# Kernel tuning notes

Hardware: AMD Instinct MI355X
Metric: run time of the kernel (lower is better)

## Reference

```python
import jax, jax.numpy as jnp
import numpy as np

HID = 2048      # hidden_size
NH = 32         # num query heads
NKV = 8         # num kv heads
HD = HID // NH  # head_dim = 64
E = 4           # num_experts
N = 2048        # flattened token count (divisible by E)
THETA = 10000.0
EPS = 1e-6


def setup_inputs() -> dict:
    key = jax.random.key(0)
    ks = jax.random.split(key, 8)
    s = HID ** -0.5
    return {
        "hidden_states": jax.random.normal(ks[0], (N, HID), jnp.float32),
        "positions": jnp.arange(N, dtype=jnp.int32),
        "sort_idx": jax.random.permutation(ks[1], N).astype(jnp.int32),
        "q_proj_w": jax.random.normal(ks[2], (E, HID, NH * HD), jnp.float32) * s,
        "o_proj_w": jax.random.normal(ks[3], (E, NH * HD, HID), jnp.float32) * s,
        "k_w": jax.random.normal(ks[4], (HID, NKV * HD), jnp.float32) * s,
        "v_w": jax.random.normal(ks[5], (HID, NKV * HD), jnp.float32) * s,
        "q_norm_w": jnp.ones((HD,), jnp.float32),
        "k_norm_w": jnp.ones((HD,), jnp.float32),
    }


def _routed_proj(x, weight, sort_idx):
    # x: [N, din], weight: [E, din, dout], sort_idx: permutation of N
    n, din = x.shape
    e, _, dout = weight.shape
    chunk = n // e
    sorted_x = x[sort_idx].reshape(e, chunk, din)          # gather + split
    sorted_out = jnp.einsum('ecd,edo->eco', sorted_x, weight).reshape(n, dout)
    return jnp.zeros((n, dout), sorted_out.dtype).at[sort_idx].set(sorted_out)


def _rms_norm(x, w):
    # x: [N, H, D] normalized over last dim
    var = jnp.mean(jnp.square(x), axis=-1, keepdims=True)
    return x * jax.lax.rsqrt(var + EPS) * w


def _rope_neox(x, positions):
    # x: [N, H, D]
    half = HD // 2
    inv_freq = 1.0 / (THETA ** (jnp.arange(0, HD, 2, dtype=jnp.float32) / HD))  # [D/2]
    freqs = positions.astype(jnp.float32)[:, None] * inv_freq                   # [N, D/2]
    cos = jnp.cos(freqs)[:, None, :]  # [N,1,D/2]
    sin = jnp.sin(freqs)[:, None, :]
    x1, x2 = x[..., :half], x[..., half:]
    return jnp.concatenate([x1 * cos - x2 * sin, x2 * cos + x1 * sin], axis=-1)


def reference(hidden_states, positions, sort_idx, q_proj_w, o_proj_w, k_w, v_w,
              q_norm_w, k_norm_w):
    n = hidden_states.shape[0]
    # projections
    q = _routed_proj(hidden_states, q_proj_w, sort_idx)        # [N, NH*HD]
    k = hidden_states @ k_w                                    # [N, NKV*HD]
    v = hidden_states @ v_w                                    # [N, NKV*HD]
    # qk norm per head
    q = _rms_norm(q.reshape(n, NH, HD), q_norm_w)
    k = _rms_norm(k.reshape(n, NKV, HD), k_norm_w)
    # rotary (neox style)
    q = _rope_neox(q, positions)
    k = _rope_neox(k, positions)
    v = v.reshape(n, NKV, HD)
    # GQA causal attention over the packed sequence
    g = NH // NKV
    k_rep = jnp.repeat(k, g, axis=1)  # [N, NH, HD]
    v_rep = jnp.repeat(v, g, axis=1)
    scores = jnp.einsum('qhd,khd->hqk', q, k_rep) * (HD ** -0.5)
    causal = positions[:, None] >= positions[None, :]          # [N, N]
    scores = jnp.where(causal[None], scores, jnp.finfo(scores.dtype).min)
    attn = jax.nn.softmax(scores, axis=-1)
    o = jnp.einsum('hqk,khd->qhd', attn, v_rep).reshape(n, NH * HD)
    # routed output projection
    return _routed_proj(o, o_proj_w, sort_idx)
```

## Files before the change

### kernel.cpp

```cpp
#include <hip/hip_runtime.h>
#include <hip/hip_bf16.h>

#define N_TOK 2048
#define HID   2048
#define NH    32
#define NKV   8
#define HD    64
#define NEXP  4
#define CHUNK (N_TOK / NEXP)
#define KV_DIM (NKV * HD)

typedef __attribute__((ext_vector_type(8))) short short8;
typedef __attribute__((ext_vector_type(4))) float float4v;

__device__ inline short f2bf(float f) {
    __hip_bfloat16 h = __float2bfloat16(f);
    return *reinterpret_cast<short*>(&h);
}
__device__ inline float bf2f(short s) {
    __hip_bfloat16 h = *reinterpret_cast<__hip_bfloat16*>(&s);
    return __bfloat162float(h);
}
__device__ __forceinline__ float fast_exp2(float x) {
    float r;
    asm("v_exp_f32 %0, %1" : "=v"(r) : "v"(x));
    return r;
}

__device__ __forceinline__ void gld_lds16(const void* g, void* l) {
    __builtin_amdgcn_global_load_lds(
        (const __attribute__((address_space(1))) unsigned int*)g,
        (__attribute__((address_space(3))) unsigned int*)l, 16, 0, 0);
}

__device__ __forceinline__ void wtrans_tile(
    const float* __restrict__ in, short* __restrict__ out, int Nw,
    int k0, int n0, float (*T)[65], int t)
{
#pragma unroll
    for (int i = 0; i < 16; i++) {
        int idx = t + i * 256, kl = idx >> 6, nl = idx & 63;
        T[kl][nl] = in[(size_t)(k0 + kl) * Nw + n0 + nl];
    }
    __syncthreads();
#pragma unroll
    for (int i = 0; i < 2; i++) {
        int idx = t + i * 256;
        int nl = idx >> 3, k8 = (idx & 7) * 8;
        short8 s;
#pragma unroll
        for (int j = 0; j < 8; j++) s[j] = f2bf(T[k8 + j][nl]);
        *(short8*)&out[(size_t)(n0 + nl) * 2048 + k0 + k8] = s;
    }
}

__global__ __launch_bounds__(256)
void prep1(const float* __restrict__ hidden, const float* __restrict__ qw,
           const float* __restrict__ kw, const float* __restrict__ vw,
           short* __restrict__ Xbf, short* __restrict__ Wq,
           short* __restrict__ Wkv)
{
    __shared__ float T[64][65];
    const int b = blockIdx.x;
    const int t = threadIdx.x;

    if (b < 2048) {
        size_t i = (size_t)b * 256 + t;
        float4 a = ((const float4*)hidden)[i * 2];
        float4 c = ((const float4*)hidden)[i * 2 + 1];
        short8 s;
        s[0] = f2bf(a.x); s[1] = f2bf(a.y); s[2] = f2bf(a.z); s[3] = f2bf(a.w);
        s[4] = f2bf(c.x); s[5] = f2bf(c.y); s[6] = f2bf(c.z); s[7] = f2bf(c.w);
        ((short8*)Xbf)[i] = s;
    } else if (b < 6144) {
        int b2 = b - 2048;
        int k0 = (b2 & 31) * 64, n0 = ((b2 >> 5) & 31) * 64, e = b2 >> 10;
        wtrans_tile(qw + (size_t)e * 2048 * 2048, Wq + (size_t)e * 2048 * 2048,
                    2048, k0, n0, T, t);
    } else {
        int b3 = b - 6144;
        int k0 = (b3 & 31) * 64, n0 = ((b3 >> 5) & 7) * 64, z = b3 >> 8;
        wtrans_tile(z ? vw : kw, Wkv + (size_t)z * 512 * 2048, 512, k0, n0, T, t);
    }
}

__global__ __launch_bounds__(256)
void prep2(const float* __restrict__ ow, short* __restrict__ Wo,
           short* __restrict__ qb, short* __restrict__ kvb,
           const float* __restrict__ qnw, const float* __restrict__ knw,
           const int* __restrict__ positions, short* __restrict__ vt)
{
    __shared__ __align__(16) char smem[64 * 65 * 4];
    const int b = blockIdx.x;
    const int t = threadIdx.x;

    if (b < 4096) {
        float (*T)[65] = (float(*)[65])smem;
        int k0 = (b & 31) * 64, n0 = ((b >> 5) & 31) * 64, e = b >> 10;
        wtrans_tile(ow + (size_t)e * 2048 * 2048, Wo + (size_t)e * 2048 * 2048,
                    2048, k0, n0, T, t);
    } else if (b < 24576) {
        const int lane = t & 63, wave = t >> 6;
        int u = (b - 4096) * 4 + wave;
        int row = u / 40, h = u - row * 40;
        short* p;
        const float* w;
        float oscale;
        if (h < NH) { p = qb + (size_t)row * 2048 + h * HD + lane; w = qnw;
                      oscale = 0.125f * 1.44269504f; }
        else        { p = kvb + (size_t)row * 1024 + (h - NH) * HD + lane; w = knw;
                      oscale = 1.0f; }
        float x = bf2f(*p);
        float ss = x * x;
#pragma unroll
        for (int off = 32; off > 0; off >>= 1) ss += __shfl_xor(ss, off, 64);
        float rs = rsqrtf(ss * (1.0f / HD) + 1e-6f);
        float xn = x * rs * w[lane];
        int j = lane & 31;
        float inv_freq = fast_exp2(-(float)j * 0.41524101186f);
        float fr = (float)positions[row] * inv_freq;
        float c = __cosf(fr), s = __sinf(fr);
        float partner = __shfl_xor(xn, 32, 64);
        float o = (lane < 32) ? (xn * c - partner * s) : (xn * c + partner * s);
        *p = f2bf(o * oscale);
    } else {
        short (*T)[66] = (short(*)[66])smem;
        int b4 = b - 24576;
        int n0 = (b4 & 31) * 64, h = b4 >> 5;
#pragma unroll
        for (int i = 0; i < 16; i++) {
            int idx = t + i * 256, nl = idx >> 6, dl = idx & 63;
            T[nl][dl] = kvb[(size_t)(n0 + nl) * 1024 + 512 + h * HD + dl];
        }
        __syncthreads();
#pragma unroll
        for (int i = 0; i < 16; i++) {
            int idx = t + i * 256, dl = idx >> 6, nl = idx & 63;
            vt[((size_t)h * HD + dl) * N_TOK + n0 + nl] = T[nl][dl];
        }
    }
}

template <bool OUT_F32>
__device__ __forceinline__ void gemm_core(
    const short* __restrict__ X, const short* __restrict__ Wt,
    const int* __restrict__ sidx, void* __restrict__ OUT,
    int dout, bool routed, int bx, int by,
    short* As0, short* Bs0, short* As1, short* Bs1, int* ridx)
{
    const int t  = threadIdx.x;
    const int m0 = by * 128;
    const int n0 = bx * 128;

    if (t < 128) ridx[t] = routed ? sidx[m0 + t] : (m0 + t);
    __syncthreads();

    const short* Wb = Wt + (routed ? (size_t)(m0 / CHUNK) * (size_t)dout * 2048 : 0);

    const int seg = (t & 3) * 8;
    const short* ga0 = X  + (size_t)ridx[t >> 2] * 2048 + seg;
    const short* ga1 = X  + (size_t)ridx[64 + (t >> 2)] * 2048 + seg;
    const short* gb0 = Wb + (size_t)(n0 + (t >> 2)) * 2048 + seg;
    const short* gb1 = Wb + (size_t)(n0 + 64 + (t >> 2)) * 2048 + seg;

    const int lane = t & 63;
    const int wave = t >> 6;
    const int wl   = wave * 64 * 8;
    const int col  = lane & 15;
    const int rowg = lane >> 4;
    const int wm   = (wave >> 1) * 64;
    const int wn   = (wave & 1) * 64;

    int offA[4], offB[4];
#pragma unroll
    for (int i = 0; i < 4; i++) {
        offA[i] = (wm + i * 16 + col) * 32 + rowg * 8;
        offB[i] = (wn + i * 16 + col) * 32 + rowg * 8;
    }

    float4v acc[4][4];
#pragma unroll
    for (int mt = 0; mt < 4; mt++)
#pragma unroll
        for (int nt = 0; nt < 4; nt++) acc[mt][nt] = (float4v){0.f, 0.f, 0.f, 0.f};

    auto stage = [&](int k0, short* A, short* B) {
        gld_lds16(ga0 + k0, A + wl);
        gld_lds16(ga1 + k0, A + 256 * 8 + wl);
        gld_lds16(gb0 + k0, B + wl);
        gld_lds16(gb1 + k0, B + 256 * 8 + wl);
    };
    auto compute = [&](const short* A, const short* B) {
        short8 af[4], bfr[4];
#pragma unroll
        for (int i = 0; i < 4; i++) af[i] = *(const short8*)&A[offA[i]];
#pragma unroll
        for (int i = 0; i < 4; i++) bfr[i] = *(const short8*)&B[offB[i]];
#pragma unroll
        for (int mt = 0; mt < 4; mt++)
#pragma unroll
            for (int nt = 0; nt < 4; nt++)
                acc[mt][nt] = __builtin_amdgcn_mfma_f32_16x16x32_bf16(
                    af[mt], bfr[nt], acc[mt][nt], 0, 0, 0);
    };

    stage(0, As0, Bs0);
    asm volatile("s_waitcnt vmcnt(0)" ::: "memory");
    __builtin_amdgcn_s_barrier();

    for (int k0 = 0; k0 < 2048; k0 += 64) {
        stage(k0 + 32, As1, Bs1);
        compute(As0, Bs0);
        asm volatile("s_waitcnt vmcnt(0)" ::: "memory");
        __builtin_amdgcn_s_barrier();

        if (k0 + 64 < 2048) stage(k0 + 64, As0, Bs0);
        compute(As1, Bs1);
        asm volatile("s_waitcnt vmcnt(0)" ::: "memory");
        __builtin_amdgcn_s_barrier();
    }

#pragma unroll
    for (int mt = 0; mt < 4; mt++) {
#pragma unroll
        for (int r = 0; r < 4; r++) {
            int row = ridx[wm + mt * 16 + rowg * 4 + r];
#pragma unroll
            for (int nt = 0; nt < 4; nt++) {
                int colg = n0 + wn + nt * 16 + col;
                float v = acc[mt][nt][r];
                if (OUT_F32) ((float*)OUT)[(size_t)row * dout + colg] = v;
                else         ((short*)OUT)[(size_t)row * dout + colg] = f2bf(v);
            }
        }
    }
}

__global__ __launch_bounds__(256)
void gemm_qkv(const short* __restrict__ X, const short* __restrict__ Wq,
              const short* __restrict__ Wkv, const int* __restrict__ sidx,
              short* __restrict__ qout, short* __restrict__ kvout)
{
    __shared__ __align__(16) short As0[128 * 32], Bs0[128 * 32];
    __shared__ __align__(16) short As1[128 * 32], Bs1[128 * 32];
    __shared__ int ridx[128];
    int b = blockIdx.x;
    if (b < 256)
        gemm_core<false>(X, Wq, sidx, qout, 2048, true, b & 15, b >> 4,
                         As0, Bs0, As1, Bs1, ridx);
    else {
        b -= 256;
        gemm_core<false>(X, Wkv, nullptr, kvout, 1024, false, b & 7, b >> 3,
                         As0, Bs0, As1, Bs1, ridx);
    }
}

__global__ __launch_bounds__(256)
void gemm_o(const short* __restrict__ X, const short* __restrict__ Wt,
            const int* __restrict__ sidx, float* __restrict__ OUT)
{
    __shared__ __align__(16) short As0[128 * 32], Bs0[128 * 32];
    __shared__ __align__(16) short As1[128 * 32], Bs1[128 * 32];
    __shared__ int ridx[128];
    gemm_core<true>(X, Wt, sidx, OUT, 2048, true, blockIdx.x, blockIdx.y,
                    As0, Bs0, As1, Bs1, ridx);
}

__global__ __launch_bounds__(256)
void attn_mfma(const short* __restrict__ qb, const short* __restrict__ kb,
               const short* __restrict__ vt, const int* __restrict__ positions,
               short* __restrict__ ob)
{
    __shared__ __align__(16) short Ks[64][72];
    __shared__ __align__(16) short Vt[64][72];
    __shared__ __align__(16) short Ps[4][16][72];

    const int head = blockIdx.y;
    const int kvh  = head >> 2;
    const int t    = threadIdx.x;
    const int lane = t & 63;
    const int wave = t >> 6;
    const int rowg = lane >> 4;
    const int col  = lane & 15;

    const int sr = t >> 2;
    const int sc = (t & 3) * 16;
    const float BIAS = 9.0f * 1.44269504f;

#pragma unroll
    for (int pass = 0; pass < 2; pass++) {
        const int qt = pass == 0 ? (31 - (int)blockIdx.x) : (int)blockIdx.x;
        const int q0 = qt * 64;
        const int m0 = q0 + wave * 16;

        const short* qrow = qb + (size_t)(m0 + col) * HID + head * HD;
        short8 aq0 = *(const short8*)(qrow + rowg * 8);
        short8 aq1 = *(const short8*)(qrow + 32 + rowg * 8);

        int pq[4];
        float l_i[4];
#pragma unroll
        for (int r = 0; r < 4; r++) {
            pq[r] = positions[m0 + rowg * 4 + r];
            l_i[r] = 0.f;
        }
        float4v oacc[4];
#pragma unroll
        for (int n = 0; n < 4; n++) oacc[n] = (float4v){0.f, 0.f, 0.f, 0.f};

        const int nkt = qt + 1;
        for (int kt = 0; kt < nkt; kt++) {
            const int k0 = kt * 64;
            __syncthreads();
            {
                const short* kp = kb + (size_t)(k0 + sr) * 1024 + kvh * HD + sc;
                const short* vp = vt + ((size_t)kvh * HD + sr) * N_TOK + k0 + sc;
                short8 kA = *(const short8*)(kp);
                short8 kB = *(const short8*)(kp + 8);
                short8 vA = *(const short8*)(vp);
                short8 vB = *(const short8*)(vp + 8);
                *(short8*)&Ks[sr][sc]     = kA;
                *(short8*)&Ks[sr][sc + 8] = kB;
                *(short8*)&Vt[sr][sc]     = vA;
                *(short8*)&Vt[sr][sc + 8] = vB;
            }
            __syncthreads();

            float4v c[4];
#pragma unroll
            for (int j = 0; j < 4; j++) {
                short8 blo = *(const short8*)&Ks[j * 16 + col][rowg * 8];
                short8 bhi = *(const short8*)&Ks[j * 16 + col][32 + rowg * 8];
                float4v cc = (float4v){0.f, 0.f, 0.f, 0.f};
                cc = __builtin_amdgcn_mfma_f32_16x16x32_bf16(aq0, blo, cc, 0, 0, 0);
                cc = __builtin_amdgcn_mfma_f32_16x16x32_bf16(aq1, bhi, cc, 0, 0, 0);
                c[j] = cc;
            }

            if (kt == qt) {
#pragma unroll
                for (int j = 0; j < 4; j++) {
                    int pk = positions[k0 + j * 16 + col];
#pragma unroll
                    for (int r = 0; r < 4; r++)
                        if (pq[r] < pk) c[j][r] = -1e30f;
                }
            }

#pragma unroll
            for (int j = 0; j < 4; j++)
#pragma unroll
                for (int r = 0; r < 4; r++) {
                    float p = fast_exp2(c[j][r] - BIAS);
                    l_i[r] += p;
                    Ps[wave][rowg * 4 + r][j * 16 + col] = f2bf(p);
                }

            __asm__ volatile("s_waitcnt lgkmcnt(0)" ::: "memory");

            short8 ap0 = *(const short8*)&Ps[wave][col][rowg * 8];
            short8 ap1 = *(const short8*)&Ps[wave][col][32 + rowg * 8];
#pragma unroll
            for (int n = 0; n < 4; n++) {
                short8 blo = *(const short8*)&Vt[n * 16 + col][rowg * 8];
                short8 bhi = *(const short8*)&Vt[n * 16 + col][32 + rowg * 8];
                float4v a2 = oacc[n];
                a2 = __builtin_amdgcn_mfma_f32_16x16x32_bf16(ap0, blo, a2, 0, 0, 0);
                a2 = __builtin_amdgcn_mfma_f32_16x16x32_bf16(ap1, bhi, a2, 0, 0, 0);
                oacc[n] = a2;
            }
        }

#pragma unroll
        for (int r = 0; r < 4; r++) {
#pragma unroll
            for (int off = 1; off < 16; off <<= 1)
                l_i[r] += __shfl_xor(l_i[r], off, 64);
            l_i[r] = 1.f / l_i[r];
        }
#pragma unroll
        for (int n = 0; n < 4; n++)
#pragma unroll
            for (int r = 0; r < 4; r++)
                ob[(size_t)(m0 + rowg * 4 + r) * HID + head * HD + n * 16 + col] =
                    f2bf(oacc[n][r] * l_i[r]);
    }
}

extern "C" void kernel_launch(void* const* d_in, const int* in_sizes, int n_in,
                              void* d_out, int out_size, void* d_ws, size_t ws_size,
                              hipStream_t stream)
{
    (void)in_sizes; (void)n_in; (void)out_size; (void)ws_size;

    const float* hidden    = (const float*)d_in[0];
    const int*   positions = (const int*)  d_in[1];
    const int*   sort_idx  = (const int*)  d_in[2];
    const float* q_proj_w  = (const float*)d_in[3];
    const float* o_proj_w  = (const float*)d_in[4];
    const float* k_w       = (const float*)d_in[5];
    const float* v_w       = (const float*)d_in[6];
    const float* q_norm_w  = (const float*)d_in[7];
    const float* k_norm_w  = (const float*)d_in[8];
    float* out = (float*)d_out;

    const size_t M1 = 1024 * 1024;
    short* Wqo = (short*)d_ws;
    short* Wkv = Wqo + 16 * M1;
    short* Xbf = Wkv + 2 * M1;
    short* qb  = Xbf + 4 * M1;
    short* kvb = qb  + 4 * M1;
    short* vt  = kvb + 2 * M1;
    short* obf = Xbf;

    prep1<<<6656, 256, 0, stream>>>(hidden, q_proj_w, k_w, v_w, Xbf, Wqo, Wkv);

    gemm_qkv<<<384, 256, 0, stream>>>(Xbf, Wqo, Wkv, sort_idx, qb, kvb);

    prep2<<<24832, 256, 0, stream>>>(o_proj_w, Wqo, qb, kvb, q_norm_w, k_norm_w,
                                     positions, vt);

    attn_mfma<<<dim3(16, NH), 256, 0, stream>>>(qb, kvb, vt, positions, obf);

    gemm_o<<<dim3(16, 16), 256, 0, stream>>>(obf, Wqo, sort_idx, out);
}
```

Measured before the change: 334.2 us.

## Fuse QK norm, RoPE and V transpose into QKV GEMM epilogue; overlap Wo transpose with attention

The separate prep2 kernel is removed. RMS norm and RoPE for q and k now run in the QKV GEMM epilogue using cross-lane shuffles, and V is written directly in transposed layout. The o_proj weight transpose is merged into the attention launch as extra blocks so it overlaps with attention, and K/V tile loads are register-prefetched one iteration ahead. This removes a full read/write pass over q, k and v and one kernel launch, at the cost of a heavier GEMM epilogue and mixed block types in the attention grid.

```diff
diff --git a/kernel.cpp b/kernel.cpp
--- a/kernel.cpp
+++ b/kernel.cpp
@@ -8,10 +8,13 @@
 #define HD    64
 #define NEXP  4
 #define CHUNK (N_TOK / NEXP)
-#define KV_DIM (NKV * HD)
 
 typedef __attribute__((ext_vector_type(8))) short short8;
+typedef __attribute__((ext_vector_type(4))) short short4v;
 typedef __attribute__((ext_vector_type(4))) float float4v;
+
+#define QSCALE (0.125f * 1.44269504f)
+#define RLOG   0.41524101186f
 
 __device__ inline short f2bf(float f) {
     __hip_bfloat16 h = __float2bfloat16(f);
@@ -84,68 +87,13 @@
     }
 }
 
-__global__ __launch_bounds__(256)
-void prep2(const float* __restrict__ ow, short* __restrict__ Wo,
-           short* __restrict__ qb, short* __restrict__ kvb,
-           const float* __restrict__ qnw, const float* __restrict__ knw,
-           const int* __restrict__ positions, short* __restrict__ vt)
-{
-    __shared__ __align__(16) char smem[64 * 65 * 4];
-    const int b = blockIdx.x;
-    const int t = threadIdx.x;
-
-    if (b < 4096) {
-        float (*T)[65] = (float(*)[65])smem;
-        int k0 = (b & 31) * 64, n0 = ((b >> 5) & 31) * 64, e = b >> 10;
-        wtrans_tile(ow + (size_t)e * 2048 * 2048, Wo + (size_t)e * 2048 * 2048,
-                    2048, k0, n0, T, t);
-    } else if (b < 24576) {
-        const int lane = t & 63, wave = t >> 6;
-        int u = (b - 4096) * 4 + wave;
-        int row = u / 40, h = u - row * 40;
-        short* p;
-        const float* w;
-        float oscale;
-        if (h < NH) { p = qb + (size_t)row * 2048 + h * HD + lane; w = qnw;
-                      oscale = 0.125f * 1.44269504f; }
-        else        { p = kvb + (size_t)row * 1024 + (h - NH) * HD + lane; w = knw;
-                      oscale = 1.0f; }
-        float x = bf2f(*p);
-        float ss = x * x;
-#pragma unroll
-        for (int off = 32; off > 0; off >>= 1) ss += __shfl_xor(ss, off, 64);
-        float rs = rsqrtf(ss * (1.0f / HD) + 1e-6f);
-        float xn = x * rs * w[lane];
-        int j = lane & 31;
-        float inv_freq = fast_exp2(-(float)j * 0.41524101186f);
-        float fr = (float)positions[row] * inv_freq;
-        float c = __cosf(fr), s = __sinf(fr);
-        float partner = __shfl_xor(xn, 32, 64);
-        float o = (lane < 32) ? (xn * c - partner * s) : (xn * c + partner * s);
-        *p = f2bf(o * oscale);
-    } else {
-        short (*T)[66] = (short(*)[66])smem;
-        int b4 = b - 24576;
-        int n0 = (b4 & 31) * 64, h = b4 >> 5;
-#pragma unroll
-        for (int i = 0; i < 16; i++) {
-            int idx = t + i * 256, nl = idx >> 6, dl = idx & 63;
-            T[nl][dl] = kvb[(size_t)(n0 + nl) * 1024 + 512 + h * HD + dl];
-        }
-        __syncthreads();
-#pragma unroll
-        for (int i = 0; i < 16; i++) {
-            int idx = t + i * 256, dl = idx >> 6, nl = idx & 63;
-            vt[((size_t)h * HD + dl) * N_TOK + n0 + nl] = T[nl][dl];
-        }
-    }
-}
-
-template <bool OUT_F32>
+template <int EPI>
 __device__ __forceinline__ void gemm_core(
     const short* __restrict__ X, const short* __restrict__ Wt,
     const int* __restrict__ sidx, void* __restrict__ OUT,
     int dout, bool routed, int bx, int by,
+    const int* __restrict__ positions, const float* __restrict__ nw,
+    short* __restrict__ vt,
     short* As0, short* Bs0, short* As1, short* Bs1, int* ridx)
 {
     const int t  = threadIdx.x;
@@ -220,38 +168,98 @@
         __builtin_amdgcn_s_barrier();
     }
 
-#pragma unroll
-    for (int mt = 0; mt < 4; mt++) {
-#pragma unroll
-        for (int r = 0; r < 4; r++) {
-            int row = ridx[wm + mt * 16 + rowg * 4 + r];
+    if (EPI == 0) {
+#pragma unroll
+        for (int mt = 0; mt < 4; mt++)
+#pragma unroll
+            for (int r = 0; r < 4; r++) {
+                int row = ridx[wm + mt * 16 + rowg * 4 + r];
+#pragma unroll
+                for (int nt = 0; nt < 4; nt++)
+                    ((float*)OUT)[(size_t)row * dout + n0 + wn + nt * 16 + col] =
+                        acc[mt][nt][r];
+            }
+        return;
+    }
+
+    const bool is_v = (EPI == 2) && (n0 + wn >= 512);
+
+    if (is_v) {
+#pragma unroll
+        for (int mt = 0; mt < 4; mt++) {
+            int rowb = m0 + wm + mt * 16 + rowg * 4;
 #pragma unroll
             for (int nt = 0; nt < 4; nt++) {
-                int colg = n0 + wn + nt * 16 + col;
-                float v = acc[mt][nt][r];
-                if (OUT_F32) ((float*)OUT)[(size_t)row * dout + colg] = v;
-                else         ((short*)OUT)[(size_t)row * dout + colg] = f2bf(v);
+                int d = n0 + wn + nt * 16 + col - 512;
+                short4v sv;
+#pragma unroll
+                for (int r = 0; r < 4; r++) sv[r] = f2bf(acc[mt][nt][r]);
+                *(short4v*)&vt[(size_t)d * N_TOK + rowb] = sv;
             }
         }
+        return;
+    }
+
+    {
+        const int   h     = (n0 + wn) >> 6;
+        const float oscl  = (EPI == 1) ? QSCALE : 1.0f;
+        const int   ldo   = (EPI == 1) ? 2048 : 512;
+        short* ob = (short*)OUT;
+        float invf0 = fast_exp2(-(float)col * RLOG);
+        float invf1 = fast_exp2(-(float)(16 + col) * RLOG);
+        float wv[4];
+#pragma unroll
+        for (int nt = 0; nt < 4; nt++) wv[nt] = nw[nt * 16 + col];
+
+#pragma unroll
+        for (int mt = 0; mt < 4; mt++)
+#pragma unroll
+            for (int r = 0; r < 4; r++) {
+                int row = ridx[wm + mt * 16 + rowg * 4 + r];
+                float x0 = acc[mt][0][r], x1 = acc[mt][1][r];
+                float x2 = acc[mt][2][r], x3 = acc[mt][3][r];
+                float ss = x0 * x0 + x1 * x1 + x2 * x2 + x3 * x3;
+#pragma unroll
+                for (int off = 1; off < 16; off <<= 1)
+                    ss += __shfl_xor(ss, off, 64);
+                float rs = rsqrtf(ss * (1.0f / HD) + 1e-6f);
+                x0 *= rs * wv[0]; x1 *= rs * wv[1];
+                x2 *= rs * wv[2]; x3 *= rs * wv[3];
+                float pos = (float)positions[row];
+                float fr0 = pos * invf0, fr1 = pos * invf1;
+                float c0 = __cosf(fr0), s0 = __sinf(fr0);
+                float c1 = __cosf(fr1), s1 = __sinf(fr1);
+                float o0 = x0 * c0 - x2 * s0;
+                float o1 = x1 * c1 - x3 * s1;
+                float o2 = x2 * c0 + x0 * s0;
+                float o3 = x3 * c1 + x1 * s1;
+                size_t base = (size_t)row * ldo + h * 64 + col;
+                ob[base]      = f2bf(o0 * oscl);
+                ob[base + 16] = f2bf(o1 * oscl);
+                ob[base + 32] = f2bf(o2 * oscl);
+                ob[base + 48] = f2bf(o3 * oscl);
+            }
     }
 }
 
 __global__ __launch_bounds__(256)
 void gemm_qkv(const short* __restrict__ X, const short* __restrict__ Wq,
               const short* __restrict__ Wkv, const int* __restrict__ sidx,
-              short* __restrict__ qout, short* __restrict__ kvout)
+              short* __restrict__ qb, short* __restrict__ kb,
+              short* __restrict__ vt, const int* __restrict__ positions,
+              const float* __restrict__ qnw, const float* __restrict__ knw)
 {
     __shared__ __align__(16) short As0[128 * 32], Bs0[128 * 32];
     __shared__ __align__(16) short As1[128 * 32], Bs1[128 * 32];
     __shared__ int ridx[128];
     int b = blockIdx.x;
     if (b < 256)
-        gemm_core<false>(X, Wq, sidx, qout, 2048, true, b & 15, b >> 4,
-                         As0, Bs0, As1, Bs1, ridx);
+        gemm_core<1>(X, Wq, sidx, qb, 2048, true, b & 15, b >> 4,
+                     positions, qnw, nullptr, As0, Bs0, As1, Bs1, ridx);
     else {
         b -= 256;
-        gemm_core<false>(X, Wkv, nullptr, kvout, 1024, false, b & 7, b >> 3,
-                         As0, Bs0, As1, Bs1, ridx);
+        gemm_core<2>(X, Wkv, nullptr, kb, 1024, false, b & 7, b >> 3,
+                     positions, knw, vt, As0, Bs0, As1, Bs1, ridx);
     }
 }
 
@@ -262,22 +270,35 @@
     __shared__ __align__(16) short As0[128 * 32], Bs0[128 * 32];
     __shared__ __align__(16) short As1[128 * 32], Bs1[128 * 32];
     __shared__ int ridx[128];
-    gemm_core<true>(X, Wt, sidx, OUT, 2048, true, blockIdx.x, blockIdx.y,
-                    As0, Bs0, As1, Bs1, ridx);
+    gemm_core<0>(X, Wt, sidx, OUT, 2048, true, blockIdx.x, blockIdx.y,
+                 nullptr, nullptr, nullptr, As0, Bs0, As1, Bs1, ridx);
 }
 
 __global__ __launch_bounds__(256)
-void attn_mfma(const short* __restrict__ qb, const short* __restrict__ kb,
+void attn_plus(const short* __restrict__ qb, const short* __restrict__ kb,
                const short* __restrict__ vt, const int* __restrict__ positions,
-               short* __restrict__ ob)
-{
-    __shared__ __align__(16) short Ks[64][72];
-    __shared__ __align__(16) short Vt[64][72];
-    __shared__ __align__(16) short Ps[4][16][72];
-
-    const int head = blockIdx.y;
+               short* __restrict__ ob,
+               const float* __restrict__ ow, short* __restrict__ Wo)
+{
+    __shared__ __align__(16) char smem[27648];
+    const int b = blockIdx.x;
+    const int t = threadIdx.x;
+
+    if (b >= 512) {
+        float (*T)[65] = (float(*)[65])smem;
+        int b2 = b - 512;
+        int k0 = (b2 & 31) * 64, n0 = ((b2 >> 5) & 31) * 64, e = b2 >> 10;
+        wtrans_tile(ow + (size_t)e * 2048 * 2048, Wo + (size_t)e * 2048 * 2048,
+                    2048, k0, n0, T, t);
+        return;
+    }
+
+    short (*Ks)[72] = (short(*)[72])smem;
+    short (*Vt)[72] = (short(*)[72])(smem + 64 * 72 * 2);
+    short (*Ps)[72] = (short(*)[72])(smem + 2 * 64 * 72 * 2);
+
+    const int head = b >> 4;
     const int kvh  = head >> 2;
-    const int t    = threadIdx.x;
     const int lane = t & 63;
     const int wave = t >> 6;
     const int rowg = lane >> 4;
@@ -289,7 +310,7 @@
 
 #pragma unroll
     for (int pass = 0; pass < 2; pass++) {
-        const int qt = pass == 0 ? (31 - (int)blockIdx.x) : (int)blockIdx.x;
+        const int qt = pass == 0 ? (31 - (b & 15)) : (b & 15);
         const int q0 = qt * 64;
         const int m0 = q0 + wave * 16;
 
@@ -308,24 +329,34 @@
 #pragma unroll
         for (int n = 0; n < 4; n++) oacc[n] = (float4v){0.f, 0.f, 0.f, 0.f};
 
+        const short* kpb = kb + (size_t)sr * 512 + kvh * HD + sc;
+        const short* vpb = vt + ((size_t)kvh * HD + sr) * N_TOK + sc;
+
         const int nkt = qt + 1;
+        short8 kA, kB, vA, vB;
+        {
+            kA = *(const short8*)(kpb);
+            kB = *(const short8*)(kpb + 8);
+            vA = *(const short8*)(vpb);
+            vB = *(const short8*)(vpb + 8);
+        }
+
         for (int kt = 0; kt < nkt; kt++) {
+            __syncthreads();
+            *(short8*)&Ks[sr][sc]     = kA;
+            *(short8*)&Ks[sr][sc + 8] = kB;
+            *(short8*)&Vt[sr][sc]     = vA;
+            *(short8*)&Vt[sr][sc + 8] = vB;
+            __syncthreads();
+
+            if (kt + 1 < nkt) {
+                kA = *(const short8*)(kpb + (size_t)(kt + 1) * 64 * 512);
+                kB = *(const short8*)(kpb + (size_t)(kt + 1) * 64 * 512 + 8);
+                vA = *(const short8*)(vpb + (kt + 1) * 64);
+                vB = *(const short8*)(vpb + (kt + 1) * 64 + 8);
+            }
+
             const int k0 = kt * 64;
-            __syncthreads();
-            {
-                const short* kp = kb + (size_t)(k0 + sr) * 1024 + kvh * HD + sc;
-                const short* vp = vt + ((size_t)kvh * HD + sr) * N_TOK + k0 + sc;
-                short8 kA = *(const short8*)(kp);
-                short8 kB = *(const short8*)(kp + 8);
-                short8 vA = *(const short8*)(vp);
-                short8 vB = *(const short8*)(vp + 8);
-                *(short8*)&Ks[sr][sc]     = kA;
-                *(short8*)&Ks[sr][sc + 8] = kB;
-                *(short8*)&Vt[sr][sc]     = vA;
-                *(short8*)&Vt[sr][sc + 8] = vB;
-            }
-            __syncthreads();
-
             float4v c[4];
 #pragma unroll
             for (int j = 0; j < 4; j++) {
@@ -353,13 +384,13 @@
                 for (int r = 0; r < 4; r++) {
                     float p = fast_exp2(c[j][r] - BIAS);
                     l_i[r] += p;
-                    Ps[wave][rowg * 4 + r][j * 16 + col] = f2bf(p);
+                    Ps[wave * 16 + rowg * 4 + r][j * 16 + col] = f2bf(p);
                 }
 
             __asm__ volatile("s_waitcnt lgkmcnt(0)" ::: "memory");
 
-            short8 ap0 = *(const short8*)&Ps[wave][col][rowg * 8];
-            short8 ap1 = *(const short8*)&Ps[wave][col][32 + rowg * 8];
+            short8 ap0 = *(const short8*)&Ps[wave * 16 + col][rowg * 8];
+            short8 ap1 = *(const short8*)&Ps[wave * 16 + col][32 + rowg * 8];
 #pragma unroll
             for (int n = 0; n < 4; n++) {
                 short8 blo = *(const short8*)&Vt[n * 16 + col][rowg * 8];
@@ -409,18 +440,17 @@
     short* Wkv = Wqo + 16 * M1;
     short* Xbf = Wkv + 2 * M1;
     short* qb  = Xbf + 4 * M1;
-    short* kvb = qb  + 4 * M1;
-    short* vt  = kvb + 2 * M1;
+    short* kb  = qb  + 4 * M1;
+    short* vt  = kb  + 1 * M1;
     short* obf = Xbf;
 
     prep1<<<6656, 256, 0, stream>>>(hidden, q_proj_w, k_w, v_w, Xbf, Wqo, Wkv);
 
-    gemm_qkv<<<384, 256, 0, stream>>>(Xbf, Wqo, Wkv, sort_idx, qb, kvb);
-
-    prep2<<<24832, 256, 0, stream>>>(o_proj_w, Wqo, qb, kvb, q_norm_w, k_norm_w,
-                                     positions, vt);
-
-    attn_mfma<<<dim3(16, NH), 256, 0, stream>>>(qb, kvb, vt, positions, obf);
+    gemm_qkv<<<384, 256, 0, stream>>>(Xbf, Wqo, Wkv, sort_idx, qb, kb, vt,
+                                      positions, q_norm_w, k_norm_w);
+
+    attn_plus<<<4608, 256, 0, stream>>>(qb, kb, vt, positions, obf,
+                                        o_proj_w, Wqo);
 
     gemm_o<<<dim3(16, 16), 256, 0, stream>>>(obf, Wqo, sort_idx, out);
 }
```

Result: faster. 298.8 us (-10.6%).
